# Kernel tuning notes

Measured on AMD Instinct MI355X. Metric: run time of the kernel, lower is better.

## Reference

```python
import jax, jax.numpy as jnp
import numpy as np

N_NODES = 100000
N_EDGES = 3200000
IN_CH = 128
HID = 16


def setup_inputs() -> dict:
    key = jax.random.key(0)
    ks = jax.random.split(key, 6)
    x = jax.random.normal(ks[0], (N_NODES, IN_CH), dtype=jnp.float32)
    edge_index = jax.random.randint(ks[1], (2, N_EDGES), 0, N_NODES, dtype=jnp.int32)
    W1 = jax.random.normal(ks[2], (IN_CH, HID), dtype=jnp.float32) / np.sqrt(IN_CH)
    b1 = jnp.zeros((HID,), jnp.float32)
    W2 = jax.random.normal(ks[3], (HID, HID), dtype=jnp.float32) / np.sqrt(HID)
    b2 = jnp.zeros((HID,), jnp.float32)
    Wl = jax.random.normal(ks[4], (HID, 1), dtype=jnp.float32) / np.sqrt(HID)
    bl = jnp.zeros((1,), jnp.float32)
    return {"x": x, "edge_index": edge_index, "W1": W1, "b1": b1,
            "W2": W2, "b2": b2, "Wl": Wl, "bl": bl}


def _gcn_conv(x, row, col, dinv, W, b, n_nodes):
    # PyG GCNConv: out[col] += d^{-1/2}[row] * d^{-1/2}[col] * (x @ W)[row]; + bias
    h = x @ W                                   # [N, C_out] small matmul
    norm = dinv[row] * dinv[col]                # [E+N] edge weights (with self-loops)
    msg = h[row] * norm[:, None]                # gather + scale
    out = jax.ops.segment_sum(msg, col, num_segments=n_nodes)  # scatter-add
    return out + b


def reference(x, edge_index, W1, b1, W2, b2, Wl, bl):
    n = x.shape[0]
    loops = jnp.arange(n, dtype=edge_index.dtype)
    row = jnp.concatenate([edge_index[0], loops])  # sources (with self-loops)
    col = jnp.concatenate([edge_index[1], loops])  # targets
    # symmetric normalization degrees computed on A + I at target index
    deg = jax.ops.segment_sum(jnp.ones(col.shape[0], x.dtype), col, num_segments=n)
    dinv = jnp.where(deg > 0, jax.lax.rsqrt(deg), 0.0)
    h = jax.nn.relu(_gcn_conv(x, row, col, dinv, W1, b1, n))
    h = jax.nn.relu(_gcn_conv(h, row, col, dinv, W2, b2, n))
    return h @ Wl + bl
```

## Files before the change

### kernel.cpp

```cpp
#include <hip/hip_runtime.h>

#define IN_CH 128
#define HID 16
#define SHIFT 8
#define BN 256
#define CAPSH 14
#define CAP (1 << CAPSH)
#define CA 16384
#define MAXNB 512
#define SCAN_B 512

typedef int vint4 __attribute__((ext_vector_type(4)));


__global__ __launch_bounds__(1024) void scatter_kernel(
    const int* __restrict__ row, const int* __restrict__ col,
    int* __restrict__ gcur, int* __restrict__ tmp, int e, int NB) {
    __shared__ int hist[MAXNB];
    __shared__ int cur[MAXNB];
    int j = blockIdx.x, t = threadIdx.x;
    for (int b = t; b < NB; b += 1024) hist[b] = 0;
    __syncthreads();
    int e4 = e >> 2;
    const int4* c4p = (const int4*)col;
    const int4* r4p = (const int4*)row;
#pragma unroll
    for (int k = 0; k < CA / 4096; ++k) {
        int i4 = j * (CA / 4) + k * 1024 + t;
        if (i4 < e4) {
            int4 c = c4p[i4];
            atomicAdd(&hist[c.x >> SHIFT], 1);
            atomicAdd(&hist[c.y >> SHIFT], 1);
            atomicAdd(&hist[c.z >> SHIFT], 1);
            atomicAdd(&hist[c.w >> SHIFT], 1);
        }
    }
    if (j == gridDim.x - 1) {
        for (int i = (e & ~3) + t; i < e; i += 1024) atomicAdd(&hist[col[i] >> SHIFT], 1);
    }
    __syncthreads();
    for (int b = t; b < NB; b += 1024) {
        int h = hist[b];
        cur[b] = (b << CAPSH) + (h ? atomicAdd(&gcur[b << 4], h) : 0);
    }
    __syncthreads();
#pragma unroll
    for (int k = 0; k < CA / 4096; ++k) {
        int i4 = j * (CA / 4) + k * 1024 + t;
        if (i4 < e4) {
            int4 c = c4p[i4];
            int4 r = r4p[i4];
            int b0, p0;
            b0 = c.x >> SHIFT; p0 = atomicAdd(&cur[b0], 1);
            if (p0 < (b0 << CAPSH) + CAP) tmp[p0] = (r.x << SHIFT) | (c.x & (BN - 1));
            b0 = c.y >> SHIFT; p0 = atomicAdd(&cur[b0], 1);
            if (p0 < (b0 << CAPSH) + CAP) tmp[p0] = (r.y << SHIFT) | (c.y & (BN - 1));
            b0 = c.z >> SHIFT; p0 = atomicAdd(&cur[b0], 1);
            if (p0 < (b0 << CAPSH) + CAP) tmp[p0] = (r.z << SHIFT) | (c.z & (BN - 1));
            b0 = c.w >> SHIFT; p0 = atomicAdd(&cur[b0], 1);
            if (p0 < (b0 << CAPSH) + CAP) tmp[p0] = (r.w << SHIFT) | (c.w & (BN - 1));
        }
    }
    if (j == gridDim.x - 1) {
        for (int i = (e & ~3) + t; i < e; i += 1024) {
            int c = col[i], r = row[i];
            int b0 = c >> SHIFT;
            int p0 = atomicAdd(&cur[b0], 1);
            if (p0 < (b0 << CAPSH) + CAP) tmp[p0] = (r << SHIFT) | (c & (BN - 1));
        }
    }
}


__global__ __launch_bounds__(512) void bucketC_kernel(
    const int* __restrict__ tmp, const int* __restrict__ gcur,
    int* __restrict__ row_ptr, int* __restrict__ pcnt, int* __restrict__ bktTot,
    float* __restrict__ dinv, int n, int NB) {
    __shared__ int hcnt[256];
    __shared__ int scn[256];
    int b = blockIdx.x, t = threadIdx.x;
    int cnt = gcur[b << 4]; if (cnt > CAP) cnt = CAP;
    int bs = b << CAPSH;
    if (t < 256) hcnt[t] = 0;
    __syncthreads();
    for (int i = t; i < cnt; i += 512) atomicAdd(&hcnt[tmp[bs + i] & (BN - 1)], 1);
    __syncthreads();
    int c = 0, pc = 0;
    if (t < 256) {
        c = hcnt[t];
        pc = (c + 7) & ~7;
        scn[t] = pc;
    }
    __syncthreads();
    for (int off = 1; off < 256; off <<= 1) {
        int a = (t >= off && t < 256) ? scn[t - off] : 0;
        __syncthreads();
        if (t < 256) scn[t] += a;
        __syncthreads();
    }
    if (t < 256) {
        int excl = scn[t] - pc;
        int node = (b << SHIFT) + t;
        if (node < n) {
            row_ptr[node] = excl;
            pcnt[node] = pc;
            dinv[node] = rsqrtf((float)(c + 1));
        }
        if (t == 255) bktTot[b] = scn[255];
    }
    if (b == 0 && t == 0) dinv[n] = 0.0f;
}

__global__ __launch_bounds__(SCAN_B) void scanB_kernel(
    int* __restrict__ bktTot, int* __restrict__ row_ptr, int NB, int n) {
    __shared__ int s[SCAN_B];
    int t = threadIdx.x;
    int v = (t < NB) ? bktTot[t] : 0;
    s[t] = v;
    __syncthreads();
    for (int off = 1; off < SCAN_B; off <<= 1) {
        int a = (t >= off) ? s[t - off] : 0;
        __syncthreads();
        s[t] += a;
        __syncthreads();
    }
    if (t < NB) bktTot[t] = s[t] - v;
    if (t == SCAN_B - 1) row_ptr[n] = s[t];
}


__global__ __launch_bounds__(512) void bucketD_kernel(
    const int* __restrict__ tmp, const int* __restrict__ gcur,
    const int* __restrict__ bktTot, const int* __restrict__ pcnt,
    int* __restrict__ row_ptr, int* __restrict__ pk, int n, int NB) {
    __shared__ int cur[256];
    int b = blockIdx.x, t = threadIdx.x;
    int cnt = gcur[b << 4]; if (cnt > CAP) cnt = CAP;
    int bs = b << CAPSH;
    int node = (b << SHIFT) + (t & 255);
    int rp = 0, pc = 0;
    if (t < 256) {
        if (node < n) {
            rp = bktTot[b] + row_ptr[node];
            pc = pcnt[node];
            row_ptr[node] = rp;
        }
        cur[t] = rp;
    }
    __syncthreads();
    for (int i = t; i < cnt; i += 512) {
        int u = tmp[bs + i];
        int pos = atomicAdd(&cur[u & (BN - 1)], 1);
        pk[pos] = u >> SHIFT;
    }
    __syncthreads();
    if (t < 256) {
        int pe = rp + pc;
        for (int p = cur[t]; p < pe; ++p) pk[p] = n;
    }
}


__global__ __launch_bounds__(256) void gemm1_kernel(
    const float* __restrict__ x, const float* __restrict__ W1,
    const float* __restrict__ dinv, float* __restrict__ hs, int n) {
    __shared__ float4 swl[512];
    int t = threadIdx.x;
#pragma unroll
    for (int i = t; i < 512; i += 256) {
        float4 v = ((const float4*)W1)[i];
        int k = i >> 2, q = i & 3;
        int kp = ((k & 31) << 2) | (k >> 5);
        swl[kp * 4 + q] = v;
    }
    __syncthreads();
    int gid = blockIdx.x * 256 + t;
    int r = gid >> 2;
    int sub = gid & 3;
    if (r > n) return;
    float4 xv[8];
    if (r < n) {
        const float4* xp = (const float4*)(x + (size_t)r * IN_CH + sub * 32);
#pragma unroll
        for (int j = 0; j < 8; ++j) xv[j] = xp[j];
    } else {
#pragma unroll
        for (int j = 0; j < 8; ++j) xv[j] = make_float4(0.f, 0.f, 0.f, 0.f);
    }
    float acc[16];
#pragma unroll
    for (int c = 0; c < 16; ++c) acc[c] = 0.f;
#pragma unroll
    for (int j = 0; j < 8; ++j) {
#pragma unroll
        for (int q = 0; q < 4; ++q) {
            int jq = j * 4 + q;
            float xs = (q == 0) ? xv[j].x : (q == 1) ? xv[j].y : (q == 2) ? xv[j].z : xv[j].w;
            const float4* wp = &swl[(jq * 4 + sub) * 4];
            float4 w0 = wp[0], w1 = wp[1], w2 = wp[2], w3 = wp[3];
            acc[0]  = fmaf(xs, w0.x, acc[0]);
            acc[1]  = fmaf(xs, w0.y, acc[1]);
            acc[2]  = fmaf(xs, w0.z, acc[2]);
            acc[3]  = fmaf(xs, w0.w, acc[3]);
            acc[4]  = fmaf(xs, w1.x, acc[4]);
            acc[5]  = fmaf(xs, w1.y, acc[5]);
            acc[6]  = fmaf(xs, w1.z, acc[6]);
            acc[7]  = fmaf(xs, w1.w, acc[7]);
            acc[8]  = fmaf(xs, w2.x, acc[8]);
            acc[9]  = fmaf(xs, w2.y, acc[9]);
            acc[10] = fmaf(xs, w2.z, acc[10]);
            acc[11] = fmaf(xs, w2.w, acc[11]);
            acc[12] = fmaf(xs, w3.x, acc[12]);
            acc[13] = fmaf(xs, w3.y, acc[13]);
            acc[14] = fmaf(xs, w3.z, acc[14]);
            acc[15] = fmaf(xs, w3.w, acc[15]);
        }
    }
#pragma unroll
    for (int c = 0; c < 16; ++c) {
        acc[c] += __shfl_xor(acc[c], 1);
        acc[c] += __shfl_xor(acc[c], 2);
    }
    float dg = (r < n) ? dinv[r] : 0.0f;
    float4 o;
    o.x = dg * acc[sub * 4 + 0];
    o.y = dg * acc[sub * 4 + 1];
    o.z = dg * acc[sub * 4 + 2];
    o.w = dg * acc[sub * 4 + 3];
    ((float4*)hs)[(size_t)r * 4 + sub] = o;
}


#define AGG_GATHER_LOOP                                                          \
    int beg = __builtin_nontemporal_load(row_ptr + node);                        \
    int end = __builtin_nontemporal_load(row_ptr + node + 1);                    \
    int j = beg + (qd << 3);                                                     \
    vint4 p0, p1;                                                                \
    if (j < end) {                                                               \
        p0 = __builtin_nontemporal_load((const vint4*)(pk + j));                 \
        p1 = __builtin_nontemporal_load((const vint4*)(pk + j + 4));             \
    }                                                                            \
    while (j < end) {                                                            \
        int jn = j + 16;                                                         \
        vint4 q0, q1;                                                            \
        if (jn < end) {                                                          \
            q0 = __builtin_nontemporal_load((const vint4*)(pk + jn));            \
            q1 = __builtin_nontemporal_load((const vint4*)(pk + jn + 4));        \
        }                                                                        \
        float4 v0 = h4[(size_t)p0.x * 4 + sub];                                  \
        float4 v1 = h4[(size_t)p0.y * 4 + sub];                                  \
        float4 v2 = h4[(size_t)p0.z * 4 + sub];                                  \
        float4 v3 = h4[(size_t)p0.w * 4 + sub];                                  \
        float4 v4 = h4[(size_t)p1.x * 4 + sub];                                  \
        float4 v5 = h4[(size_t)p1.y * 4 + sub];                                  \
        float4 v6 = h4[(size_t)p1.z * 4 + sub];                                  \
        float4 v7 = h4[(size_t)p1.w * 4 + sub];                                  \
        cx += ((v0.x + v1.x) + (v2.x + v3.x)) + ((v4.x + v5.x) + (v6.x + v7.x)); \
        cy += ((v0.y + v1.y) + (v2.y + v3.y)) + ((v4.y + v5.y) + (v6.y + v7.y)); \
        cz += ((v0.z + v1.z) + (v2.z + v3.z)) + ((v4.z + v5.z) + (v6.z + v7.z)); \
        cw += ((v0.w + v1.w) + (v2.w + v3.w)) + ((v4.w + v5.w) + (v6.w + v7.w)); \
        p0 = q0; p1 = q1; j = jn;                                                \
    }                                                                            \
    cx += __shfl_xor(cx, 4);                                                     \
    cy += __shfl_xor(cy, 4);                                                     \
    cz += __shfl_xor(cz, 4);                                                     \
    cw += __shfl_xor(cw, 4);

__global__ __launch_bounds__(256) void agg1_kernel(
    const float* __restrict__ hs, const int* __restrict__ row_ptr,
    const int* __restrict__ pk, const float* __restrict__ dinv,
    const float* __restrict__ b1, const float* __restrict__ W2,
    float* __restrict__ hs2, int n) {
    int t = threadIdx.x;
    int node = blockIdx.x * 32 + (t >> 3);
    int sub = t & 3;
    int qd  = (t >> 2) & 1;
    if (node >= n) return;
    const float4* h4 = (const float4*)hs;
    float4 self = h4[(size_t)node * 4 + sub];
    float cx = qd ? 0.f : self.x, cy = qd ? 0.f : self.y;
    float cz = qd ? 0.f : self.z, cw = qd ? 0.f : self.w;
    AGG_GATHER_LOOP
    float dg = dinv[node];
    float4 b1v = *(const float4*)(b1 + (sub << 2));
    float ax = fmaxf(fmaf(dg, cx, b1v.x), 0.f);
    float ay = fmaxf(fmaf(dg, cy, b1v.y), 0.f);
    float az = fmaxf(fmaf(dg, cz, b1v.z), 0.f);
    float aw = fmaxf(fmaf(dg, cw, b1v.w), 0.f);
    float ox = 0.f, oy = 0.f, oz = 0.f, ow = 0.f;
#pragma unroll
    for (int r = 0; r < 4; ++r) {
        float fx = __shfl_xor(ax, r);
        float fy = __shfl_xor(ay, r);
        float fz = __shfl_xor(az, r);
        float fw = __shfl_xor(aw, r);
        int kb = (sub ^ r) << 2;
        const float* wp = W2 + kb * HID + (sub << 2);
        float4 w0 = *(const float4*)(wp);
        float4 w1 = *(const float4*)(wp + HID);
        float4 w2 = *(const float4*)(wp + 2 * HID);
        float4 w3 = *(const float4*)(wp + 3 * HID);
        ox += fx * w0.x + fy * w1.x + fz * w2.x + fw * w3.x;
        oy += fx * w0.y + fy * w1.y + fz * w2.y + fw * w3.y;
        oz += fx * w0.z + fy * w1.z + fz * w2.z + fw * w3.z;
        ow += fx * w0.w + fy * w1.w + fz * w2.w + fw * w3.w;
    }
    if (qd == 0) {
        float4 o; o.x = dg * ox; o.y = dg * oy; o.z = dg * oz; o.w = dg * ow;
        ((float4*)hs2)[(size_t)node * 4 + sub] = o;
    }
}

__global__ __launch_bounds__(256) void agg2_kernel(
    const float* __restrict__ hs2, const int* __restrict__ row_ptr,
    const int* __restrict__ pk, const float* __restrict__ dinv,
    const float* __restrict__ b2, const float* __restrict__ Wl,
    const float* __restrict__ bl, float* __restrict__ out, int n) {
    int t = threadIdx.x;
    int node = blockIdx.x * 32 + (t >> 3);
    int sub = t & 3;
    int qd  = (t >> 2) & 1;
    if (node >= n) return;
    const float4* h4 = (const float4*)hs2;
    float4 self = h4[(size_t)node * 4 + sub];
    float cx = qd ? 0.f : self.x, cy = qd ? 0.f : self.y;
    float cz = qd ? 0.f : self.z, cw = qd ? 0.f : self.w;
    AGG_GATHER_LOOP
    float dg = dinv[node];
    float4 b2v = *(const float4*)(b2 + (sub << 2));
    float4 wlv = *(const float4*)(Wl + (sub << 2));
    float p = fmaxf(fmaf(dg, cx, b2v.x), 0.f) * wlv.x
            + fmaxf(fmaf(dg, cy, b2v.y), 0.f) * wlv.y
            + fmaxf(fmaf(dg, cz, b2v.z), 0.f) * wlv.z
            + fmaxf(fmaf(dg, cw, b2v.w), 0.f) * wlv.w;
    p += __shfl_xor(p, 1);
    p += __shfl_xor(p, 2);
    if ((t & 7) == 0) out[node] = p + bl[0];
}

extern "C" void kernel_launch(void* const* d_in, const int* in_sizes, int n_in,
                              void* d_out, int out_size, void* d_ws, size_t ws_size,
                              hipStream_t stream) {
    const float* x  = (const float*)d_in[0];
    const int*   ei = (const int*)d_in[1];
    const float* W1 = (const float*)d_in[2];
    const float* b1 = (const float*)d_in[3];
    const float* W2 = (const float*)d_in[4];
    const float* b2 = (const float*)d_in[5];
    const float* Wl = (const float*)d_in[6];
    const float* bl = (const float*)d_in[7];

    int n = in_sizes[0] / IN_CH;
    int e = in_sizes[1] / 2;
    const int* row = ei;
    const int* col = ei + e;

    int NB  = (n + BN - 1) >> SHIFT;
    int nba = (e + CA - 1) / CA;

    char* ws = (char*)d_ws;
    size_t off = 0;
    auto alloc = [&](size_t bytes) -> void* {
        void* p = ws + off;
        off = (off + bytes + 255) & ~(size_t)255;
        return p;
    };

    size_t tabf = (size_t)(n + 1) * HID;

    int*   gcur    = (int*)alloc((size_t)NB * 16 * 4);
    int*   tmp     = (int*)alloc(((size_t)NB << CAPSH) * 4);
    int*   row_ptr = (int*)alloc(((size_t)n + 1) * 4);
    int*   pcnt    = (int*)alloc((size_t)n * 4);
    int*   bktTot  = (int*)alloc((size_t)NB * 4);
    float* dinv    = (float*)alloc(((size_t)n + 1) * 4);
    int*   pk      = (int*)alloc(((size_t)e + 8 * (size_t)n + 64) * 4);
    float* hs      = (float*)alloc(tabf * 4);
    float* hs2     = (float*)alloc(tabf * 4);

    dim3 gG((4 * (n + 1) + 255) / 256);
    dim3 gA((8 * n + 255) / 256);

    (void)hipMemsetAsync(gcur, 0, (size_t)NB * 16 * 4, stream);
    (void)hipMemsetAsync(hs2 + (size_t)n * HID, 0, HID * 4, stream);
    hipLaunchKernelGGL(scatter_kernel, dim3(nba), dim3(1024), 0, stream, row, col, gcur, tmp, e, NB);
    hipLaunchKernelGGL(bucketC_kernel, dim3(NB),  dim3(512),  0, stream, tmp, gcur, row_ptr, pcnt, bktTot, dinv, n, NB);
    hipLaunchKernelGGL(scanB_kernel,   dim3(1),   dim3(SCAN_B), 0, stream, bktTot, row_ptr, NB, n);
    hipLaunchKernelGGL(bucketD_kernel, dim3(NB),  dim3(512),  0, stream, tmp, gcur, bktTot, pcnt, row_ptr, pk, n, NB);

    hipLaunchKernelGGL(gemm1_kernel, gG, dim3(256), 0, stream, x, W1, dinv, hs, n);
    hipLaunchKernelGGL(agg1_kernel,  gA, dim3(256), 0, stream, hs, row_ptr, pk, dinv, b1, W2, hs2, n);
    hipLaunchKernelGGL(agg2_kernel,  gA, dim3(256), 0, stream, hs2, row_ptr, pk, dinv, b2, Wl, bl, (float*)d_out, n);
}
```

Baseline: 149.1 us.

## Fuse bucket count and CSR fill in place, drop global bucket scan

Merges the bucket histogram kernel, the single-block bucket-offset scan and the bucket fill kernel into one kernel. Each block stages its bucket slab in a 64 KB LDS buffer, builds per-node offsets, and writes the padded neighbour lists back into its own slab of tmp instead of a separate compacted pk array. Since slabs are no longer contiguous, the aggregation kernels now read a separate per-node end pointer (pend) instead of row_ptr[node+1]. This removes two launches, the global scan and one re-read of tmp. In exchange the large LDS footprint limits occupancy, and a slab could overflow if padded counts exceed CAP.

Result: faster. 143.8 us (-3.5%).

```diff
diff --git a/kernel.cpp b/kernel.cpp
--- a/kernel.cpp
+++ b/kernel.cpp
@@ -8,7 +8,6 @@
 #define CAP (1 << CAPSH)
 #define CA 16384
 #define MAXNB 512
-#define SCAN_B 512
 
 typedef int vint4 __attribute__((ext_vector_type(4)));
 
@@ -72,18 +71,21 @@
 }
 
 
-__global__ __launch_bounds__(512) void bucketC_kernel(
-    const int* __restrict__ tmp, const int* __restrict__ gcur,
-    int* __restrict__ row_ptr, int* __restrict__ pcnt, int* __restrict__ bktTot,
+__global__ __launch_bounds__(512) void bucketCD_kernel(
+    int* __restrict__ tmp, const int* __restrict__ gcur,
+    int* __restrict__ row_ptr, int* __restrict__ pend,
     float* __restrict__ dinv, int n, int NB) {
+    __shared__ int sbuf[CAP];
     __shared__ int hcnt[256];
     __shared__ int scn[256];
+    __shared__ int cur[256];
     int b = blockIdx.x, t = threadIdx.x;
     int cnt = gcur[b << 4]; if (cnt > CAP) cnt = CAP;
     int bs = b << CAPSH;
     if (t < 256) hcnt[t] = 0;
-    __syncthreads();
-    for (int i = t; i < cnt; i += 512) atomicAdd(&hcnt[tmp[bs + i] & (BN - 1)], 1);
+    for (int i = t; i < cnt; i += 512) sbuf[i] = tmp[bs + i];
+    __syncthreads();
+    for (int i = t; i < cnt; i += 512) atomicAdd(&hcnt[sbuf[i] & (BN - 1)], 1);
     __syncthreads();
     int c = 0, pc = 0;
     if (t < 256) {
@@ -98,65 +100,28 @@
         if (t < 256) scn[t] += a;
         __syncthreads();
     }
+    int rp = 0;
     if (t < 256) {
-        int excl = scn[t] - pc;
+        rp = bs + scn[t] - pc;
         int node = (b << SHIFT) + t;
         if (node < n) {
-            row_ptr[node] = excl;
-            pcnt[node] = pc;
+            row_ptr[node] = rp;
+            pend[node] = rp + pc;
             dinv[node] = rsqrtf((float)(c + 1));
         }
-        if (t == 255) bktTot[b] = scn[255];
+        cur[t] = rp;
     }
     if (b == 0 && t == 0) dinv[n] = 0.0f;
-}
-
-__global__ __launch_bounds__(SCAN_B) void scanB_kernel(
-    int* __restrict__ bktTot, int* __restrict__ row_ptr, int NB, int n) {
-    __shared__ int s[SCAN_B];
-    int t = threadIdx.x;
-    int v = (t < NB) ? bktTot[t] : 0;
-    s[t] = v;
-    __syncthreads();
-    for (int off = 1; off < SCAN_B; off <<= 1) {
-        int a = (t >= off) ? s[t - off] : 0;
-        __syncthreads();
-        s[t] += a;
-        __syncthreads();
-    }
-    if (t < NB) bktTot[t] = s[t] - v;
-    if (t == SCAN_B - 1) row_ptr[n] = s[t];
-}
-
-
-__global__ __launch_bounds__(512) void bucketD_kernel(
-    const int* __restrict__ tmp, const int* __restrict__ gcur,
-    const int* __restrict__ bktTot, const int* __restrict__ pcnt,
-    int* __restrict__ row_ptr, int* __restrict__ pk, int n, int NB) {
-    __shared__ int cur[256];
-    int b = blockIdx.x, t = threadIdx.x;
-    int cnt = gcur[b << 4]; if (cnt > CAP) cnt = CAP;
-    int bs = b << CAPSH;
-    int node = (b << SHIFT) + (t & 255);
-    int rp = 0, pc = 0;
-    if (t < 256) {
-        if (node < n) {
-            rp = bktTot[b] + row_ptr[node];
-            pc = pcnt[node];
-            row_ptr[node] = rp;
-        }
-        cur[t] = rp;
-    }
     __syncthreads();
     for (int i = t; i < cnt; i += 512) {
-        int u = tmp[bs + i];
+        int u = sbuf[i];
         int pos = atomicAdd(&cur[u & (BN - 1)], 1);
-        pk[pos] = u >> SHIFT;
+        tmp[pos] = u >> SHIFT;
     }
     __syncthreads();
     if (t < 256) {
         int pe = rp + pc;
-        for (int p = cur[t]; p < pe; ++p) pk[p] = n;
+        for (int p = cur[t]; p < pe; ++p) tmp[p] = n;
     }
 }
 
@@ -233,7 +198,7 @@
 
 #define AGG_GATHER_LOOP                                                          \
     int beg = __builtin_nontemporal_load(row_ptr + node);                        \
-    int end = __builtin_nontemporal_load(row_ptr + node + 1);                    \
+    int end = __builtin_nontemporal_load(pend + node);                           \
     int j = beg + (qd << 3);                                                     \
     vint4 p0, p1;                                                                \
     if (j < end) {                                                               \
@@ -268,7 +233,8 @@
 
 __global__ __launch_bounds__(256) void agg1_kernel(
     const float* __restrict__ hs, const int* __restrict__ row_ptr,
-    const int* __restrict__ pk, const float* __restrict__ dinv,
+    const int* __restrict__ pend, const int* __restrict__ pk,
+    const float* __restrict__ dinv,
     const float* __restrict__ b1, const float* __restrict__ W2,
     float* __restrict__ hs2, int n) {
     int t = threadIdx.x;
@@ -313,7 +279,8 @@
 
 __global__ __launch_bounds__(256) void agg2_kernel(
     const float* __restrict__ hs2, const int* __restrict__ row_ptr,
-    const int* __restrict__ pk, const float* __restrict__ dinv,
+    const int* __restrict__ pend, const int* __restrict__ pk,
+    const float* __restrict__ dinv,
     const float* __restrict__ b2, const float* __restrict__ Wl,
     const float* __restrict__ bl, float* __restrict__ out, int n) {
     int t = threadIdx.x;
@@ -370,11 +337,9 @@
 
     int*   gcur    = (int*)alloc((size_t)NB * 16 * 4);
     int*   tmp     = (int*)alloc(((size_t)NB << CAPSH) * 4);
-    int*   row_ptr = (int*)alloc(((size_t)n + 1) * 4);
-    int*   pcnt    = (int*)alloc((size_t)n * 4);
-    int*   bktTot  = (int*)alloc((size_t)NB * 4);
+    int*   row_ptr = (int*)alloc((size_t)n * 4);
+    int*   pend    = (int*)alloc((size_t)n * 4);
     float* dinv    = (float*)alloc(((size_t)n + 1) * 4);
-    int*   pk      = (int*)alloc(((size_t)e + 8 * (size_t)n + 64) * 4);
     float* hs      = (float*)alloc(tabf * 4);
     float* hs2     = (float*)alloc(tabf * 4);
 
@@ -383,12 +348,10 @@
 
     (void)hipMemsetAsync(gcur, 0, (size_t)NB * 16 * 4, stream);
     (void)hipMemsetAsync(hs2 + (size_t)n * HID, 0, HID * 4, stream);
-    hipLaunchKernelGGL(scatter_kernel, dim3(nba), dim3(1024), 0, stream, row, col, gcur, tmp, e, NB);
-    hipLaunchKernelGGL(bucketC_kernel, dim3(NB),  dim3(512),  0, stream, tmp, gcur, row_ptr, pcnt, bktTot, dinv, n, NB);
-    hipLaunchKernelGGL(scanB_kernel,   dim3(1),   dim3(SCAN_B), 0, stream, bktTot, row_ptr, NB, n);
-    hipLaunchKernelGGL(bucketD_kernel, dim3(NB),  dim3(512),  0, stream, tmp, gcur, bktTot, pcnt, row_ptr, pk, n, NB);
+    hipLaunchKernelGGL(scatter_kernel,  dim3(nba), dim3(1024), 0, stream, row, col, gcur, tmp, e, NB);
+    hipLaunchKernelGGL(bucketCD_kernel, dim3(NB),  dim3(512),  0, stream, tmp, gcur, row_ptr, pend, dinv, n, NB);
 
     hipLaunchKernelGGL(gemm1_kernel, gG, dim3(256), 0, stream, x, W1, dinv, hs, n);
-    hipLaunchKernelGGL(agg1_kernel,  gA, dim3(256), 0, stream, hs, row_ptr, pk, dinv, b1, W2, hs2, n);
-    hipLaunchKernelGGL(agg2_kernel,  gA, dim3(256), 0, stream, hs2, row_ptr, pk, dinv, b2, Wl, bl, (float*)d_out, n);
-}
+    hipLaunchKernelGGL(agg1_kernel,  gA, dim3(256), 0, stream, hs, row_ptr, pend, tmp, dinv, b1, W2, hs2, n);
+    hipLaunchKernelGGL(agg2_kernel,  gA, dim3(256), 0, stream, hs2, row_ptr, pend, tmp, dinv, b2, Wl, bl, (float*)d_out, n);
+}
```
